# Kernel tuning notes

Measured on AMD Instinct MI355X. Metric: run time of the kernel, lower is better.

Reference implementation:

```python
import jax, jax.numpy as jnp
import numpy as np

B, R, T, N = 64, 2, 32, 128
C_IN, C_OUT = 64, 64
PRELU_INIT = 0.25


def setup_inputs() -> dict:
    key = jax.random.key(0)
    ks = jax.random.split(key, 6)
    x = jax.random.normal(ks[0], (B, C_IN, T, N), dtype=jnp.float32)
    A = jax.random.uniform(ks[1], (B, R, T, N, N), dtype=jnp.float32)  # non-negative adjacency
    # per-relation 1x1 conv (t_kernel_size=1, relation=1 per gcn since split=[])
    w_gcn = jax.random.normal(ks[2], (R, C_OUT, C_IN), dtype=jnp.float32) * (1.0 / np.sqrt(C_IN))
    b_gcn = jnp.zeros((R, C_OUT), dtype=jnp.float32)
    # tcn temporal conv: kernel (3,1), padding (1,0)
    w_tcn = jax.random.normal(ks[3], (C_OUT, C_OUT, 3, 1), dtype=jnp.float32) * (1.0 / np.sqrt(3 * C_OUT))
    b_tcn = jnp.zeros((C_OUT,), dtype=jnp.float32)
    a_tcn = jnp.float32(PRELU_INIT)  # PReLU inside tcn
    a_out = jnp.float32(PRELU_INIT)  # final PReLU
    return {"x": x, "A": A, "w_gcn": w_gcn, "b_gcn": b_gcn,
            "w_tcn": w_tcn, "b_tcn": b_tcn, "a_tcn": a_tcn, "a_out": a_out}


def _prelu(x, a):
    return jnp.where(x >= 0, x, a * x)


def _normalized_laplacian_tilde(A):
    # A: (..., N, N); A_tilde = A + I, return D^{-1/2} A_tilde D^{-1/2}
    n = A.shape[-1]
    A_t = A + jnp.eye(n, dtype=A.dtype)
    d_inv_sqrt = jax.lax.rsqrt(A_t.sum(-1))  # (..., N); rowsum >= 1
    return d_inv_sqrt[..., :, None] * A_t * d_inv_sqrt[..., None, :]


def reference(x, A, w_gcn, b_gcn, w_tcn, b_tcn, a_tcn, a_out):
    # x: (B,C,T,N), A: (B,R,T,N,N). Eval mode: drop_edge is identity, dropout inactive.
    res = x  # in_channels == out_channels, stride == 1
    # per-relation 1x1 convs, batched over R
    x_c = jnp.einsum('bctn,roc->brotn', x, w_gcn) + b_gcn[None, :, :, None, None]
    A_norm = _normalized_laplacian_tilde(A)  # (B,R,T,N,N)
    # bmm per (r,t): out[b,c,m] = sum_n x_c[b,r,c,t,n] * A_norm[b,r,t,n,m], summed over r
    x_comb = jnp.einsum('brctn,brtnm->bctm', x_c, A_norm)
    # tcn: PReLU -> Conv2d (3,1) pad (1,0) -> Dropout(0)
    h = _prelu(x_comb, a_tcn)
    h = jax.lax.conv_general_dilated(
        h, w_tcn, window_strides=(1, 1), padding=((1, 1), (0, 0)),
        dimension_numbers=('NCHW', 'OIHW', 'NCHW'))
    h = h + b_tcn[None, :, None, None]
    out = _prelu(h + res, a_out)
    return (out, A)
```

## Files before the change

kernel.cpp:

```cpp
#include <hip/hip_runtime.h>
#include <hip/hip_bf16.h>

typedef unsigned short u16;
typedef unsigned int u32;
typedef __attribute__((ext_vector_type(8))) short bf16x8;
typedef __attribute__((ext_vector_type(4))) float f32x4;
typedef __attribute__((ext_vector_type(4))) u16 u16x4;
typedef __attribute__((ext_vector_type(8))) u16 u16x8;

#define B_ 64
#define R_ 2
#define T_ 32
#define N_ 128
#define C_ 64

__device__ __forceinline__ u16 f2bf(float f) {
  return __builtin_bit_cast(u16, __float2bfloat16(f));
}
__device__ __forceinline__ float bf2f(u16 h) {
  u32 u = ((u32)h) << 16;
  return __builtin_bit_cast(float, u);
}

#define MFMA __builtin_amdgcn_mfma_f32_16x16x32_bf16

#define STG16(gsrc, ldst)                                                   \
  __builtin_amdgcn_global_load_lds(                                         \
      (const __attribute__((address_space(1))) u32*)(gsrc),                 \
      (__attribute__((address_space(3))) u32*)(ldst), 16, 0, 0)

#define BAR()                                                  \
  do {                                                         \
    asm volatile("s_waitcnt lgkmcnt(0)" ::: "memory");         \
    __builtin_amdgcn_s_barrier();                              \
    __builtin_amdgcn_sched_barrier(0);                         \
  } while (0)

#define WAITVM(N)                                              \
  do {                                                         \
    asm volatile("s_waitcnt vmcnt(" #N ")" ::: "memory");      \
    __builtin_amdgcn_sched_barrier(0);                         \
  } while (0)

__device__ __forceinline__ void gl_chunk(const float* Abase, float* rb,
                                         int w, int lane) {
#pragma unroll
  for (int g = 0; g < 4; ++g) {
    const int d = (w * 4 + g) * 64 + lane;
    const int c4 = d >> 5;
    const int rl = (d & 31) ^ (c4 & 7);
    STG16(Abase + rl * 128 + c4 * 4, rb + (w * 4 + g) * 256);
  }
}

__device__ __forceinline__ void consume(const float* rb, int ch,
                                        u16 (*ATb)[32], float* outAs,
                                        float* dscr, int tid, float4* gv) {
  const int c4 = tid & 31, rb8 = tid >> 5;
  const float4* rf4 = (const float4*)rb;
#pragma unroll
  for (int j = 0; j < 4; ++j)
    gv[j] = rf4[c4 * 32 + (((rb8 << 2) + j) ^ (c4 & 7))];
  float d4[4];
#pragma unroll
  for (int j = 0; j < 4; ++j) {
    float s = (gv[j].x + gv[j].y) + (gv[j].z + gv[j].w);
    s += __shfl_xor(s, 1); s += __shfl_xor(s, 2); s += __shfl_xor(s, 4);
    s += __shfl_xor(s, 8); s += __shfl_xor(s, 16);
    d4[j] = rsqrtf(s + 1.0f);
  }
  if (c4 == 0) {
    float4 dv = {d4[0], d4[1], d4[2], d4[3]};
    *(float4*)(dscr + ch * 32 + rb8 * 4) = dv;
  }
#pragma unroll
  for (int j = 0; j < 4; ++j)
    *(float4*)(outAs + (size_t)(ch * 32 + rb8 * 4 + j) * N_ + c4 * 4) = gv[j];
  const int nb = (rb8 << 2) ^ ((c4 & 7) << 2);
#pragma unroll
  for (int i = 0; i < 4; ++i) {
    const int m = c4 * 4 + i;
    u16x4 pk;
#pragma unroll
    for (int j = 0; j < 4; ++j) {
      float v = ((const float*)&gv[j])[i];
      if (m == ch * 32 + rb8 * 4 + j) v += 1.0f;
      pk[j] = f2bf(v * d4[j]);
    }
    *(u16x4*)&ATb[m][nb] = pk;
  }
}

__device__ __forceinline__ void load_wg(bf16x8 wf[2][2], const float* wg, int r,
                                        int wr, int lr, int lg) {
#pragma unroll
  for (int kk = 0; kk < 2; ++kk)
#pragma unroll
    for (int mr = 0; mr < 2; ++mr) {
      const float* p = wg + ((size_t)(r * C_ + 32 * wr + 16 * mr + lr)) * C_ + 32 * kk + 8 * lg;
      float4 a = *(const float4*)p, b = *(const float4*)(p + 4);
      bf16x8 f;
      f[0] = (short)f2bf(a.x); f[1] = (short)f2bf(a.y);
      f[2] = (short)f2bf(a.z); f[3] = (short)f2bf(a.w);
      f[4] = (short)f2bf(b.x); f[5] = (short)f2bf(b.y);
      f[6] = (short)f2bf(b.z); f[7] = (short)f2bf(b.w);
      wf[kk][mr] = f;
    }
}

__device__ __forceinline__ void mm1f(u16 (*TMP)[128], const bf16x8 wf[2][2],
                                     const bf16x8 bfr[2][4], const float4 bias[2],
                                     int wr, int wc, int lr, int lg) {
  f32x4 acc1[2][4] = {};
#pragma unroll
  for (int kk = 0; kk < 2; ++kk)
#pragma unroll
    for (int mr = 0; mr < 2; ++mr)
#pragma unroll
      for (int nc = 0; nc < 4; ++nc)
        acc1[mr][nc] = MFMA(wf[kk][mr], bfr[kk][nc], acc1[mr][nc], 0, 0, 0);
#pragma unroll
  for (int mr = 0; mr < 2; ++mr) {
    const int o0 = 32 * wr + 16 * mr + 4 * lg;
    const float bb[4] = {bias[mr].x, bias[mr].y, bias[mr].z, bias[mr].w};
#pragma unroll
    for (int nc = 0; nc < 4; ++nc) {
      const int n = 64 * wc + 16 * nc + lr;
#pragma unroll
      for (int i = 0; i < 4; ++i)
        TMP[o0 + i][n ^ (i << 4)] = f2bf(acc1[mr][nc][i] + bb[i]);
    }
  }
}

__device__ __forceinline__ void mm2k(f32x4 acc[2][4], const u16 (*TMP)[128],
                                     const u16 (*ATb)[32], int ch,
                                     int wr, int wc, int lr, int lg) {
  bf16x8 af[2], bfr[4];
#pragma unroll
  for (int mr = 0; mr < 2; ++mr) {
    const int c = 32 * wr + 16 * mr + lr;
    const int colT = (ch * 32 + 8 * lg) ^ ((lr & 3) << 4);
    af[mr] = *(const bf16x8*)&TMP[c][colT];
  }
#pragma unroll
  for (int nc = 0; nc < 4; ++nc) {
    const int m = 64 * wc + 16 * nc + lr;
    const int swz = ((m >> 2) & 7) << 2;
    const int base = (8 * lg) ^ (swz & 24);
    const int s4 = swz & 4;
    u16x4 h0 = *(const u16x4*)&ATb[m][base + s4];
    u16x4 h1 = *(const u16x4*)&ATb[m][base + (4 ^ s4)];
    bf16x8 f;
    f[0] = (short)h0[0]; f[1] = (short)h0[1]; f[2] = (short)h0[2]; f[3] = (short)h0[3];
    f[4] = (short)h1[0]; f[5] = (short)h1[1]; f[6] = (short)h1[2]; f[7] = (short)h1[3];
    bfr[nc] = f;
  }
#pragma unroll
  for (int mr = 0; mr < 2; ++mr)
#pragma unroll
    for (int nc = 0; nc < 4; ++nc)
      acc[mr][nc] = MFMA(af[mr], bfr[nc], acc[mr][nc], 0, 0, 0);
}

__global__ __launch_bounds__(256, 2) void k_gcn(
    const float* __restrict__ x, const float* __restrict__ A,
    const float* __restrict__ wg, const float* __restrict__ bg,
    float* __restrict__ outA, u16* __restrict__ wsX, float* __restrict__ dscrg) {
  __shared__ __align__(16) float RB[3][32 * 128];
  __shared__ __align__(16) u16 AT[2][N_][32];
  __shared__ __align__(16) u16 TMP[C_][128];

  const int tid = threadIdx.x;
  const int bid = ((blockIdx.x & 7) << 8) | (blockIdx.x >> 3);
  const int b = bid >> 5, t = bid & 31;
  const int lane = tid & 63, w = tid >> 6;
  const int wr = w >> 1, wc = w & 1;
  const int lr = lane & 15, lg = lane >> 4;

  const size_t Asl0 = ((size_t)((b * R_ + 0) * T_ + t)) * (size_t)(N_ * N_);
  const size_t Asl1 = ((size_t)((b * R_ + 1) * T_ + t)) * (size_t)(N_ * N_);
  float* dscr = dscrg + (size_t)bid * 256;

  float4 xv[8];
  {
    const int c = tid & 63, ub = tid >> 6;
    const float* xp = x + ((size_t)(b * C_ + c) * T_ + t) * N_ + 32 * ub;
#pragma unroll
    for (int j = 0; j < 8; ++j) xv[j] = *(const float4*)(xp + 4 * j);
  }
  bf16x8 wf0[2][2], wf1[2][2];
  load_wg(wf0, wg, 0, wr, lr, lg);
  load_wg(wf1, wg, 1, wr, lr, lg);
  float4 bias[R_][2];
#pragma unroll
  for (int r = 0; r < R_; ++r)
#pragma unroll
    for (int mr = 0; mr < 2; ++mr)
      bias[r][mr] = *(const float4*)(bg + r * C_ + 32 * wr + 16 * mr + 4 * lg);
  gl_chunk(A + Asl0, RB[0], w, lane);
  gl_chunk(A + Asl0 + 4096, RB[1], w, lane);
  __builtin_amdgcn_sched_barrier(0);

  u16 (*XT)[64] = (u16(*)[64])RB[2];
  {
    const int c = tid & 63, ub = tid >> 6;
#pragma unroll
    for (int j = 0; j < 8; ++j) {
      const int n0 = 32 * ub + 4 * j;
      XT[n0 + 0][c] = f2bf(xv[j].x);
      XT[n0 + 1][c ^ 16] = f2bf(xv[j].y);
      XT[n0 + 2][c ^ 32] = f2bf(xv[j].z);
      XT[n0 + 3][c ^ 48] = f2bf(xv[j].w);
    }
  }
  BAR();

  f32x4 accA[2][4] = {};
  f32x4 accB[2][4] = {};
  float4 gvA[4], gvB[4];

  bf16x8 bfrx[2][4];
#pragma unroll
  for (int kk = 0; kk < 2; ++kk)
#pragma unroll
    for (int nc = 0; nc < 4; ++nc) {
      const int n = 64 * wc + 16 * nc + lr;
      const int col = (32 * kk + 8 * lg) ^ ((lr & 3) << 4);
      bfrx[kk][nc] = *(const bf16x8*)&XT[n][col];
    }
  mm1f(TMP, wf0, bfrx, bias[0], wr, wc, lr, lg);
  WAITVM(4);
  consume(RB[0], 0, AT[0], outA + Asl0, dscr, tid, gvA);
  BAR();

  gl_chunk(A + Asl0 + 8192, RB[2], w, lane);
  mm2k(accA, TMP, AT[0], 0, wr, wc, lr, lg);
  WAITVM(4);
  consume(RB[1], 1, AT[1], outA + Asl0, dscr, tid, gvB);
  BAR();

  gl_chunk(A + Asl0 + 12288, RB[0], w, lane);
  mm2k(accA, TMP, AT[1], 1, wr, wc, lr, lg);
  WAITVM(4);
  consume(RB[2], 2, AT[0], outA + Asl0, dscr, tid, gvA);
  BAR();

  gl_chunk(A + Asl1, RB[1], w, lane);
  mm2k(accA, TMP, AT[0], 2, wr, wc, lr, lg);
  WAITVM(4);
  consume(RB[0], 3, AT[1], outA + Asl0, dscr, tid, gvB);
  BAR();

  gl_chunk(A + Asl1 + 4096, RB[2], w, lane);
  mm2k(accA, TMP, AT[1], 3, wr, wc, lr, lg);
  WAITVM(4);
  consume(RB[1], 0, AT[0], outA + Asl1, dscr + 128, tid, gvA);
  BAR();

  gl_chunk(A + Asl1 + 8192, RB[0], w, lane);
  mm1f(TMP, wf1, bfrx, bias[1], wr, wc, lr, lg);
  WAITVM(4);
  consume(RB[2], 1, AT[1], outA + Asl1, dscr + 128, tid, gvB);
  BAR();

  gl_chunk(A + Asl1 + 12288, RB[1], w, lane);
  mm2k(accB, TMP, AT[0], 0, wr, wc, lr, lg);
  BAR();

  mm2k(accB, TMP, AT[1], 1, wr, wc, lr, lg);
  WAITVM(4);
  consume(RB[0], 2, AT[0], outA + Asl1, dscr + 128, tid, gvA);
  BAR();

  mm2k(accB, TMP, AT[0], 2, wr, wc, lr, lg);
  WAITVM(0);
  consume(RB[1], 3, AT[1], outA + Asl1, dscr + 128, tid, gvB);
  BAR();

  mm2k(accB, TMP, AT[1], 3, wr, wc, lr, lg);
  WAITVM(0);
  BAR();

  float dA[4], dB[4];
#pragma unroll
  for (int nc = 0; nc < 4; ++nc) {
    const int m = 64 * wc + 16 * nc + lr;
    dA[nc] = dscr[m];
    dB[nc] = dscr[128 + m];
  }
  u16* stage = &TMP[0][0];
#pragma unroll
  for (int mr = 0; mr < 2; ++mr)
#pragma unroll
    for (int nc = 0; nc < 4; ++nc) {
      const int m = 64 * wc + 16 * nc + lr;
      const int c0 = 32 * wr + 16 * mr + 4 * lg;
#pragma unroll
      for (int i = 0; i < 4; ++i) {
        const float v = dA[nc] * accA[mr][nc][i] + dB[nc] * accB[mr][nc][i];
        stage[m * 64 + ((c0 + i) ^ ((m & 7) << 3))] = f2bf(v);
      }
    }
  BAR();
  {
    u16* wp = wsX + ((size_t)(b * T_ + t) * N_) * C_;
#pragma unroll
    for (int it = 0; it < 4; ++it) {
      const int idx = it * 2048 + tid * 8;
      const int m = idx >> 6, a = idx & 63;
      u16x8 v = *(const u16x8*)&stage[m * 64 + a];
      *(u16x8*)(wp + m * 64 + (a ^ ((m & 7) << 3))) = v;
    }
  }
}

__global__ __launch_bounds__(256, 3) void k_tcn(
    const u16* __restrict__ wsX, const float* __restrict__ x,
    const float* __restrict__ wt, const float* __restrict__ bt,
    const float* __restrict__ a_tcn, const float* __restrict__ a_out,
    float* __restrict__ out) {
  __shared__ __align__(16) u16 HT[N_][200];
  const int tid = threadIdx.x;
  const int bid = ((blockIdx.x & 7) << 8) | (blockIdx.x >> 3);
  const int b = bid >> 5, t = bid & 31;
  const int lane = tid & 63, wv = tid >> 6;
  const int wr = wv >> 1, wc = wv & 1;
  const int lr = lane & 15, lg = lane >> 4;
  const float at = a_tcn[0], ao = a_out[0];

  bf16x8 wfr[6][2];
#pragma unroll
  for (int kq = 0; kq < 6; ++kq) {
    const int dt = kq >> 1;
    const int ci0 = (32 * kq + 8 * lg) & 63;
#pragma unroll
    for (int mr = 0; mr < 2; ++mr) {
      const int co = 32 * wr + 16 * mr + lr;
      const float* p = wt + ((size_t)co * C_ + ci0) * 3 + dt;
      float e[8];
#pragma unroll
      for (int j = 0; j < 8; ++j) e[j] = p[3 * j];
      bf16x8 f;
#pragma unroll
      for (int j = 0; j < 8; ++j) f[j] = (short)f2bf(e[j]);
      wfr[kq][mr] = f;
    }
  }

#pragma unroll
  for (int dt = 0; dt < 3; ++dt) {
    const int t2 = t + dt - 1;
    const bool ok = (t2 >= 0) && (t2 < T_);
    const u16* p = wsX + ((size_t)(b * T_ + (ok ? t2 : 0)) * N_) * C_;
    u16x8 hv[4];
#pragma unroll
    for (int i3 = 0; i3 < 4; ++i3) {
      const int idx = i3 * 256 + tid;
      const int n = idx >> 3, c8 = (idx & 7) * 8;
      u16x8 z = {0, 0, 0, 0, 0, 0, 0, 0};
      hv[i3] = ok ? *(const u16x8*)(p + n * C_ + c8) : z;
    }
#pragma unroll
    for (int i3 = 0; i3 < 4; ++i3) {
      const int idx = i3 * 256 + tid;
      const int n = idx >> 3, c8 = (idx & 7) * 8;
      u16x8 o;
#pragma unroll
      for (int j = 0; j < 8; ++j) {
        float f = bf2f((u16)hv[i3][j]);
        o[j] = f2bf(f < 0.f ? at * f : f);
      }
      *(u16x8*)&HT[n][dt * 64 + c8] = o;
    }
  }
  __syncthreads();

  f32x4 acc[2][4] = {};
#pragma unroll
  for (int kq = 0; kq < 6; ++kq) {
    bf16x8 bfr[4];
#pragma unroll
    for (int nc = 0; nc < 4; ++nc)
      bfr[nc] = *(const bf16x8*)&HT[64 * wc + 16 * nc + lr][32 * kq + 8 * lg];
#pragma unroll
    for (int mr = 0; mr < 2; ++mr)
#pragma unroll
      for (int nc = 0; nc < 4; ++nc)
        acc[mr][nc] = MFMA(wfr[kq][mr], bfr[nc], acc[mr][nc], 0, 0, 0);
  }

#pragma unroll
  for (int mr = 0; mr < 2; ++mr) {
    const int co0 = 32 * wr + 16 * mr + 4 * lg;
    float bts[4];
#pragma unroll
    for (int i = 0; i < 4; ++i) bts[i] = bt[co0 + i];
#pragma unroll
    for (int nc = 0; nc < 4; ++nc) {
      const int n = 64 * wc + 16 * nc + lr;
#pragma unroll
      for (int i = 0; i < 4; ++i) {
        const size_t gi = ((size_t)(b * C_ + co0 + i) * T_ + t) * N_ + n;
        float v = acc[mr][nc][i] + bts[i] + x[gi];
        out[gi] = (v < 0.f) ? ao * v : v;
      }
    }
  }
}

extern "C" void kernel_launch(void* const* d_in, const int* in_sizes, int n_in,
                              void* d_out, int out_size, void* d_ws, size_t ws_size,
                              hipStream_t stream) {
  const float* x = (const float*)d_in[0];
  const float* A = (const float*)d_in[1];
  const float* wg = (const float*)d_in[2];
  const float* bg = (const float*)d_in[3];
  const float* wt = (const float*)d_in[4];
  const float* bt = (const float*)d_in[5];
  const float* atc = (const float*)d_in[6];
  const float* aoc = (const float*)d_in[7];
  float* out = (float*)d_out;
  float* outA = out + (size_t)B_ * C_ * T_ * N_;
  u16* wsX = (u16*)d_ws;
  float* dscr = out;

  k_gcn<<<B_ * T_, 256, 0, stream>>>(x, A, wg, bg, outA, wsX, dscr);
  k_tcn<<<B_ * T_, 256, 0, stream>>>(wsX, x, wt, bt, atc, aoc, out);
}
```

Measured before the change: 206.1 us.

## Coalesce adjacency chunk loads and precompute both relation projections upfront

Adjacency chunk loads now read contiguous global addresses and use a plain row-major LDS layout instead of the XOR-swizzled transposed pattern, with the consumer's LDS indexing updated to match. This targets uncoalesced global reads of A. The staging ring shrinks from three buffers to two, and the freed LDS holds a second TMP buffer, so both per-relation 1x1 projections are computed before the A pipeline starts. In exchange, only one A chunk is prefetched ahead instead of two, which may expose more memory latency. The final mm2k also moves past the last barrier.

```diff
diff --git a/kernel.cpp b/kernel.cpp
--- a/kernel.cpp
+++ b/kernel.cpp
@@ -47,9 +47,7 @@
 #pragma unroll
   for (int g = 0; g < 4; ++g) {
     const int d = (w * 4 + g) * 64 + lane;
-    const int c4 = d >> 5;
-    const int rl = (d & 31) ^ (c4 & 7);
-    STG16(Abase + rl * 128 + c4 * 4, rb + (w * 4 + g) * 256);
+    STG16(Abase + d * 4, rb + (w * 4 + g) * 256);
   }
 }
 
@@ -60,7 +58,7 @@
   const float4* rf4 = (const float4*)rb;
 #pragma unroll
   for (int j = 0; j < 4; ++j)
-    gv[j] = rf4[c4 * 32 + (((rb8 << 2) + j) ^ (c4 & 7))];
+    gv[j] = rf4[((rb8 << 2) + j) * 32 + c4];
   float d4[4];
 #pragma unroll
   for (int j = 0; j < 4; ++j) {
@@ -167,9 +165,9 @@
     const float* __restrict__ x, const float* __restrict__ A,
     const float* __restrict__ wg, const float* __restrict__ bg,
     float* __restrict__ outA, u16* __restrict__ wsX, float* __restrict__ dscrg) {
-  __shared__ __align__(16) float RB[3][32 * 128];
+  __shared__ __align__(16) float RB[2][4096];
   __shared__ __align__(16) u16 AT[2][N_][32];
-  __shared__ __align__(16) u16 TMP[C_][128];
+  __shared__ __align__(16) u16 TMP[2][C_][128];
 
   const int tid = threadIdx.x;
   const int bid = ((blockIdx.x & 7) << 8) | (blockIdx.x >> 3);
@@ -199,10 +197,9 @@
     for (int mr = 0; mr < 2; ++mr)
       bias[r][mr] = *(const float4*)(bg + r * C_ + 32 * wr + 16 * mr + 4 * lg);
   gl_chunk(A + Asl0, RB[0], w, lane);
-  gl_chunk(A + Asl0 + 4096, RB[1], w, lane);
   __builtin_amdgcn_sched_barrier(0);
 
-  u16 (*XT)[64] = (u16(*)[64])RB[2];
+  u16 (*XT)[64] = (u16(*)[64])RB[1];
   {
     const int c = tid & 63, ub = tid >> 6;
 #pragma unroll
@@ -229,81 +226,84 @@
       const int col = (32 * kk + 8 * lg) ^ ((lr & 3) << 4);
       bfrx[kk][nc] = *(const bf16x8*)&XT[n][col];
     }
-  mm1f(TMP, wf0, bfrx, bias[0], wr, wc, lr, lg);
+  mm1f(TMP[0], wf0, bfrx, bias[0], wr, wc, lr, lg);
+  mm1f(TMP[1], wf1, bfrx, bias[1], wr, wc, lr, lg);
+  BAR();
+
+  gl_chunk(A + Asl0 + 4096, RB[1], w, lane);
   WAITVM(4);
   consume(RB[0], 0, AT[0], outA + Asl0, dscr, tid, gvA);
   BAR();
 
-  gl_chunk(A + Asl0 + 8192, RB[2], w, lane);
-  mm2k(accA, TMP, AT[0], 0, wr, wc, lr, lg);
+  gl_chunk(A + Asl0 + 8192, RB[0], w, lane);
+  mm2k(accA, TMP[0], AT[0], 0, wr, wc, lr, lg);
   WAITVM(4);
   consume(RB[1], 1, AT[1], outA + Asl0, dscr, tid, gvB);
   BAR();
 
-  gl_chunk(A + Asl0 + 12288, RB[0], w, lane);
-  mm2k(accA, TMP, AT[1], 1, wr, wc, lr, lg);
-  WAITVM(4);
-  consume(RB[2], 2, AT[0], outA + Asl0, dscr, tid, gvA);
-  BAR();
-
-  gl_chunk(A + Asl1, RB[1], w, lane);
-  mm2k(accA, TMP, AT[0], 2, wr, wc, lr, lg);
-  WAITVM(4);
-  consume(RB[0], 3, AT[1], outA + Asl0, dscr, tid, gvB);
-  BAR();
-
-  gl_chunk(A + Asl1 + 4096, RB[2], w, lane);
-  mm2k(accA, TMP, AT[1], 3, wr, wc, lr, lg);
-  WAITVM(4);
-  consume(RB[1], 0, AT[0], outA + Asl1, dscr + 128, tid, gvA);
+  gl_chunk(A + Asl0 + 12288, RB[1], w, lane);
+  mm2k(accA, TMP[0], AT[1], 1, wr, wc, lr, lg);
+  WAITVM(4);
+  consume(RB[0], 2, AT[0], outA + Asl0, dscr, tid, gvA);
+  BAR();
+
+  gl_chunk(A + Asl1, RB[0], w, lane);
+  mm2k(accA, TMP[0], AT[0], 2, wr, wc, lr, lg);
+  WAITVM(4);
+  consume(RB[1], 3, AT[1], outA + Asl0, dscr, tid, gvB);
+  BAR();
+
+  gl_chunk(A + Asl1 + 4096, RB[1], w, lane);
+  mm2k(accA, TMP[0], AT[1], 3, wr, wc, lr, lg);
+  WAITVM(4);
+  consume(RB[0], 0, AT[0], outA + Asl1, dscr + 128, tid, gvA);
   BAR();
 
   gl_chunk(A + Asl1 + 8192, RB[0], w, lane);
-  mm1f(TMP, wf1, bfrx, bias[1], wr, wc, lr, lg);
-  WAITVM(4);
-  consume(RB[2], 1, AT[1], outA + Asl1, dscr + 128, tid, gvB);
+  mm2k(accB, TMP[1], AT[0], 0, wr, wc, lr, lg);
+  WAITVM(4);
+  consume(RB[1], 1, AT[1], outA + Asl1, dscr + 128, tid, gvB);
   BAR();
 
   gl_chunk(A + Asl1 + 12288, RB[1], w, lane);
-  mm2k(accB, TMP, AT[0], 0, wr, wc, lr, lg);
-  BAR();
-
-  mm2k(accB, TMP, AT[1], 1, wr, wc, lr, lg);
+  mm2k(accB, TMP[1], AT[1], 1, wr, wc, lr, lg);
   WAITVM(4);
   consume(RB[0], 2, AT[0], outA + Asl1, dscr + 128, tid, gvA);
   BAR();
 
-  mm2k(accB, TMP, AT[0], 2, wr, wc, lr, lg);
+  mm2k(accB, TMP[1], AT[0], 2, wr, wc, lr, lg);
   WAITVM(0);
   consume(RB[1], 3, AT[1], outA + Asl1, dscr + 128, tid, gvB);
-  BAR();
-
-  mm2k(accB, TMP, AT[1], 3, wr, wc, lr, lg);
   WAITVM(0);
   BAR();
 
-  float dA[4], dB[4];
-#pragma unroll
-  for (int nc = 0; nc < 4; ++nc) {
-    const int m = 64 * wc + 16 * nc + lr;
-    dA[nc] = dscr[m];
-    dB[nc] = dscr[128 + m];
-  }
-  u16* stage = &TMP[0][0];
-#pragma unroll
-  for (int mr = 0; mr < 2; ++mr)
+  mm2k(accB, TMP[1], AT[1], 3, wr, wc, lr, lg);
+  {
+    float dA[4], dB[4];
 #pragma unroll
     for (int nc = 0; nc < 4; ++nc) {
       const int m = 64 * wc + 16 * nc + lr;
-      const int c0 = 32 * wr + 16 * mr + 4 * lg;
-#pragma unroll
-      for (int i = 0; i < 4; ++i) {
-        const float v = dA[nc] * accA[mr][nc][i] + dB[nc] * accB[mr][nc][i];
-        stage[m * 64 + ((c0 + i) ^ ((m & 7) << 3))] = f2bf(v);
+      dA[nc] = dscr[m];
+      dB[nc] = dscr[128 + m];
+    }
+    u16* stage = &TMP[0][0][0];
+#pragma unroll
+    for (int mr = 0; mr < 2; ++mr)
+#pragma unroll
+      for (int nc = 0; nc < 4; ++nc) {
+        const int m = 64 * wc + 16 * nc + lr;
+        const int c0 = 32 * wr + 16 * mr + 4 * lg;
+#pragma unroll
+        for (int i = 0; i < 4; ++i) {
+          const float v = dA[nc] * accA[mr][nc][i] + dB[nc] * accB[mr][nc][i];
+          stage[m * 64 + ((c0 + i) ^ ((m & 7) << 3))] = f2bf(v);
+        }
       }
-    }
-  BAR();
+  }
+  BAR();
+
   {
+    const u16* stage = &TMP[0][0][0];
     u16* wp = wsX + ((size_t)(b * T_ + t) * N_) * C_;
 #pragma unroll
     for (int it = 0; it < 4; ++it) {
```

After: 201.4 us. 2.3% less time.
